# Kernel optimization log

Hardware: AMD Instinct MI355X
Metric: run time of the kernel (lower is better)

Reference implementation:

```python
import jax, jax.numpy as jnp
import numpy as np

P_W, P_H = 4, 8            # patch_size=[4,8]: p[0]=width, p[1]=height
EMBED, DEPTH, HEADS = 384, 12, 6
HD = EMBED // HEADS        # 64
THETA = 100.0
LN_EPS = 1e-5


def axial_freqs(pw, ph):
    # compute_axial_cis(dim=HD, end_x=pw, end_y=ph): angles for x and y axes, as cos/sin
    f = 1.0 / THETA ** (np.arange(0, HD, 4)[: HD // 4].astype(np.float32) / HD)  # (16,)
    t = np.arange(pw * ph, dtype=np.float32)
    tx, ty = t % pw, np.floor(t / pw)
    ang = np.concatenate([np.outer(tx, f), np.outer(ty, f)], -1)  # (N, 32)
    return jnp.asarray(np.cos(ang)), jnp.asarray(np.sin(ang))


def patchify(img):
    # (3, h, w) -> (ph*pw, 3*P_H*P_W), matching view/permute in NaViT_ROPE.forward
    c, h, w = img.shape
    ph, pw = h // P_H, w // P_W
    seq = img.reshape(c, ph, P_H, pw, P_W).transpose(1, 3, 0, 2, 4).reshape(ph * pw, -1)
    return seq, ph, pw


def layer_norm(x, w, b):
    m = x.mean(-1, keepdims=True)
    v = ((x - m) ** 2).mean(-1, keepdims=True)
    return (x - m) / jnp.sqrt(v + LN_EPS) * w + b


def rope(x, cos, sin):
    # x: (B,H,N,HD) paired as (...,HD//2,2); cos/sin: (B,N,HD//2)
    xp = x.reshape(*x.shape[:-1], -1, 2)
    x0, x1 = xp[..., 0], xp[..., 1]
    c, s = cos[:, None], sin[:, None]
    return jnp.stack([x0 * c - x1 * s, x0 * s + x1 * c], -1).reshape(x.shape)


def forward(imgs, params):
    (pe_ln_in_w, pe_ln_in_b, pe_w, pe_ln_out_w, pe_ln_out_b, blk, lnf_w, lnf_b) = params
    seqs, coss, sins, lens = [], [], [], []
    for img in imgs:
        seq, ph, pw = patchify(img)
        c, s = axial_freqs(pw, ph)
        seqs.append(seq); coss.append(c); sins.append(s); lens.append(seq.shape[0])
    nmax = max(lens)
    pad = lambda a: jnp.pad(a, ((0, nmax - a.shape[0]), (0, 0)))
    x = jnp.stack([pad(s) for s in seqs])      # (B, Nmax, 96)
    cos = jnp.stack([pad(c) for c in coss])    # (B, Nmax, 32)
    sin = jnp.stack([pad(s) for s in sins])
    mask = jnp.arange(nmax)[None, :] >= jnp.array(lens)[:, None]        # (B, Nmax), True = pad
    attn_bias = jnp.where(mask, -jnp.inf, 0.0)[:, None, None, :]        # (B,1,1,Nmax)

    # patch embed: LN(96) -> Linear(96,384,no bias) -> LN(384)
    x = layer_norm(x, pe_ln_in_w, pe_ln_in_b) @ pe_w
    x = layer_norm(x, pe_ln_out_w, pe_ln_out_b)

    scale = HD ** -0.5

    def block(x, p):
        ln1_w, ln1_b, qkv_w, qkv_b, proj_w, proj_b, ln2_w, ln2_b, fc1_w, fc1_b, fc2_w, fc2_b = p
        B, N, C = x.shape
        h = layer_norm(x, ln1_w, ln1_b)
        qkv = (h @ qkv_w + qkv_b).reshape(B, N, 3, HEADS, HD).transpose(2, 0, 3, 1, 4)
        q, k, v = qkv[0], qkv[1], qkv[2]
        q, k = rope(q, cos, sin), rope(k, cos, sin)
        attn = jnp.einsum('bhnd,bhmd->bhnm', q * scale, k) + attn_bias
        attn = jax.nn.softmax(attn, axis=-1)
        o = jnp.einsum('bhnm,bhmd->bhnd', attn, v).transpose(0, 2, 1, 3).reshape(B, N, C)
        x = x + (o @ proj_w + proj_b)
        h2 = layer_norm(x, ln2_w, ln2_b)
        h2 = jax.nn.gelu(h2 @ fc1_w + fc1_b, approximate=False)  # torch nn.GELU default (erf)
        x = x + (h2 @ fc2_w + fc2_b)
        return x, None

    x, _ = jax.lax.scan(block, x, blk)
    x = layer_norm(x, lnf_w, lnf_b)
    return x, mask


def setup_inputs() -> dict:
    key = jax.random.key(0)
    ks = jax.random.split(key, 10)
    sizes = [(3, 32, 512), (3, 32, 768), (3, 32, 896), (3, 32, 1024)]
    pd = 3 * P_H * P_W  # 96
    w = lambda k, sh: jax.random.normal(k, sh, jnp.float32) * 0.02
    inp = {}
    for i, s in enumerate(sizes):
        inp[f'img{i}'] = jax.random.normal(ks[i], s, jnp.float32)
    inp.update(
        pe_ln_in_w=jnp.ones((pd,), jnp.float32), pe_ln_in_b=jnp.zeros((pd,), jnp.float32),
        pe_w=w(ks[4], (pd, EMBED)),
        pe_ln_out_w=jnp.ones((EMBED,), jnp.float32), pe_ln_out_b=jnp.zeros((EMBED,), jnp.float32),
        ln1_w=jnp.ones((DEPTH, EMBED), jnp.float32), ln1_b=jnp.zeros((DEPTH, EMBED), jnp.float32),
        qkv_w=w(ks[5], (DEPTH, EMBED, 3 * EMBED)), qkv_b=jnp.zeros((DEPTH, 3 * EMBED), jnp.float32),
        proj_w=w(ks[6], (DEPTH, EMBED, EMBED)), proj_b=jnp.zeros((DEPTH, EMBED), jnp.float32),
        ln2_w=jnp.ones((DEPTH, EMBED), jnp.float32), ln2_b=jnp.zeros((DEPTH, EMBED), jnp.float32),
        fc1_w=w(ks[7], (DEPTH, EMBED, 4 * EMBED)), fc1_b=jnp.zeros((DEPTH, 4 * EMBED), jnp.float32),
        fc2_w=w(ks[8], (DEPTH, 4 * EMBED, EMBED)), fc2_b=jnp.zeros((DEPTH, EMBED), jnp.float32),
        lnf_w=jnp.ones((EMBED,), jnp.float32), lnf_b=jnp.zeros((EMBED,), jnp.float32),
    )
    return inp


def reference(img0, img1, img2, img3, pe_ln_in_w, pe_ln_in_b, pe_w, pe_ln_out_w, pe_ln_out_b,
              ln1_w, ln1_b, qkv_w, qkv_b, proj_w, proj_b, ln2_w, ln2_b,
              fc1_w, fc1_b, fc2_w, fc2_b, lnf_w, lnf_b):
    blk = (ln1_w, ln1_b, qkv_w, qkv_b, proj_w, proj_b, ln2_w, ln2_b, fc1_w, fc1_b, fc2_w, fc2_b)
    return forward([img0, img1, img2, img3],
                   (pe_ln_in_w, pe_ln_in_b, pe_w, pe_ln_out_w, pe_ln_out_b, blk, lnf_w, lnf_b))
```

## Files before the change

kernel.cpp:

```cpp
#include <hip/hip_runtime.h>


#define EMBED 384
#define NHEADS 6
#define HD 64
#define NSEQ 1024
#define NB 4
#define NROWS (NB * NSEQ)
#define PD 96

typedef __attribute__((ext_vector_type(8))) short bf16x8;
typedef __attribute__((ext_vector_type(4))) float f32x4;

__constant__ int c_lens[4] = {512, 768, 896, 1024};

__device__ __forceinline__ unsigned f2bf(float f) {
    unsigned u = __float_as_uint(f);
    return (u + 0x7fffu + ((u >> 16) & 1u)) >> 16;
}
__device__ __forceinline__ float bf2f(unsigned short h) {
    return __uint_as_float(((unsigned)h) << 16);
}

__global__ void patchify_kernel(const float* __restrict__ i0, const float* __restrict__ i1,
                                const float* __restrict__ i2, const float* __restrict__ i3,
                                float* __restrict__ xin, float* __restrict__ cosT,
                                float* __restrict__ sinT) {
    int bn = blockIdx.x;
    int b = bn >> 10, n = bn & 1023;
    const int lens[4] = {512, 768, 896, 1024};
    const int pws[4]  = {128, 192, 224, 256};
    const float* imgs[4] = {i0, i1, i2, i3};
    int len = lens[b], pw = pws[b];
    int W = pw * 4;
    int t = threadIdx.x;
    float* xrow = xin + (size_t)bn * PD;
    if (n < len) {
        int pr = n / pw, pc = n - pr * pw;
        const float* img = imgs[b];
        if (t < PD) {
            int c = t >> 5, py = (t >> 2) & 7, px = t & 3;
            xrow[t] = img[(size_t)c * 32 * W + (size_t)(pr * 8 + py) * W + pc * 4 + px];
        }
        if (t < 32) {
            int j = t & 15;
            float fr = powf(100.0f, -(float)j / 16.0f);
            float coord = (t < 16) ? (float)pc : (float)pr;
            float ang = coord * fr;
            cosT[(size_t)bn * 32 + t] = cosf(ang);
            sinT[(size_t)bn * 32 + t] = sinf(ang);
        }
    } else {
        if (t < PD) xrow[t] = 0.f;
        if (t < 32) { cosT[(size_t)bn * 32 + t] = 0.f; sinT[(size_t)bn * 32 + t] = 0.f; }
    }
}

__global__ void convT_kernel(const float* __restrict__ src, unsigned short* __restrict__ dst,
                             int K, int N, int Kpad) {
    __shared__ float tile[32][33];
    int k0 = blockIdx.x * 32, n0 = blockIdx.y * 32, l = blockIdx.z;
    int t = threadIdx.x;
    {
        int kk = t >> 3, nn = (t & 7) * 4;
        float4 v = make_float4(0.f, 0.f, 0.f, 0.f);
        if (k0 + kk < K)
            v = *(const float4*)(src + ((size_t)l * K + (k0 + kk)) * N + n0 + nn);
        tile[kk][nn + 0] = v.x; tile[kk][nn + 1] = v.y;
        tile[kk][nn + 2] = v.z; tile[kk][nn + 3] = v.w;
    }
    __syncthreads();
    {
        int nn = t >> 3, kk = (t & 7) * 4;
        unsigned lo = f2bf(tile[kk + 0][nn]) | (f2bf(tile[kk + 1][nn]) << 16);
        unsigned hi = f2bf(tile[kk + 2][nn]) | (f2bf(tile[kk + 3][nn]) << 16);
        uint2 u = make_uint2(lo, hi);
        *(uint2*)(dst + (size_t)l * N * Kpad + (size_t)(n0 + nn) * Kpad + k0 + kk) = u;
    }
}

template <int C, int OS, bool OBF>
__global__ void ln_kernel(const float* __restrict__ in, const float* __restrict__ w,
                          const float* __restrict__ bias, void* __restrict__ outv) {
    int row = blockIdx.x * 4 + (threadIdx.x >> 6);
    int t = threadIdx.x & 63;
    const float* x = in + (size_t)row * C;
    constexpr int NE = (C + 63) / 64;
    float vals[NE];
    float s = 0.f;
#pragma unroll
    for (int i = 0; i < NE; i++) {
        int e = t + i * 64;
        float v = (e < C) ? x[e] : 0.f;
        vals[i] = v; s += v;
    }
#pragma unroll
    for (int off = 32; off; off >>= 1) s += __shfl_down(s, off);
    float mean = __shfl(s, 0) / (float)C;
    float vs = 0.f;
#pragma unroll
    for (int i = 0; i < NE; i++) {
        int e = t + i * 64;
        float d = (e < C) ? (vals[i] - mean) : 0.f;
        vs += d * d;
    }
#pragma unroll
    for (int off = 32; off; off >>= 1) vs += __shfl_down(vs, off);
    float rstd = rsqrtf(__shfl(vs, 0) / (float)C + 1e-5f);
    constexpr int NO = (OS + 63) / 64;
#pragma unroll
    for (int i = 0; i < NO; i++) {
        int e = t + i * 64;
        if (e < OS) {
            float v = (e < C) ? ((vals[i] - mean) * rstd * w[e] + bias[e]) : 0.f;
            if (OBF) ((unsigned short*)outv)[(size_t)row * OS + e] = (unsigned short)f2bf(v);
            else     ((float*)outv)[(size_t)row * OS + e] = v;
        }
    }
}

template <int FLAGS>
__global__ __launch_bounds__(256) void gemm_bf16(
    const unsigned short* __restrict__ A, const unsigned short* __restrict__ Wt,
    const float* __restrict__ bias, const float* __restrict__ res,
    float* __restrict__ outf, unsigned short* __restrict__ outb,
    int M, int K, int N) {
    __shared__ unsigned short As[64][72];
    __shared__ unsigned short Bs[64][72];
    int t = threadIdx.x;
    int wid = t >> 6, lane = t & 63;
    int m0 = blockIdx.y * 64, n0 = blockIdx.x * 64;
    int wm = (wid >> 1) * 32, wn = (wid & 1) * 32;
    f32x4 acc[2][2] = {};
    int srow = t >> 2, sc = (t & 3) * 8;
    const unsigned short* Ap = A + (size_t)(m0 + srow) * K + sc;
    const unsigned short* Bp = Wt + (size_t)(n0 + srow) * K + sc;
    int lr = lane & 15, lk = (lane >> 4) * 8;
    for (int k0 = 0; k0 < K; k0 += 64) {
        *(uint4*)&As[srow][sc]      = *(const uint4*)(Ap + k0);
        *(uint4*)&As[srow][sc + 32] = *(const uint4*)(Ap + k0 + 32);
        *(uint4*)&Bs[srow][sc]      = *(const uint4*)(Bp + k0);
        *(uint4*)&Bs[srow][sc + 32] = *(const uint4*)(Bp + k0 + 32);
        __syncthreads();
#pragma unroll
        for (int kk = 0; kk < 64; kk += 32) {
            bf16x8 a0 = *(const bf16x8*)&As[wm + lr][kk + lk];
            bf16x8 a1 = *(const bf16x8*)&As[wm + 16 + lr][kk + lk];
            bf16x8 b0 = *(const bf16x8*)&Bs[wn + lr][kk + lk];
            bf16x8 b1 = *(const bf16x8*)&Bs[wn + 16 + lr][kk + lk];
            acc[0][0] = __builtin_amdgcn_mfma_f32_16x16x32_bf16(a0, b0, acc[0][0], 0, 0, 0);
            acc[0][1] = __builtin_amdgcn_mfma_f32_16x16x32_bf16(a0, b1, acc[0][1], 0, 0, 0);
            acc[1][0] = __builtin_amdgcn_mfma_f32_16x16x32_bf16(a1, b0, acc[1][0], 0, 0, 0);
            acc[1][1] = __builtin_amdgcn_mfma_f32_16x16x32_bf16(a1, b1, acc[1][1], 0, 0, 0);
        }
        __syncthreads();
    }
    int lq = lane >> 4;
#pragma unroll
    for (int mi = 0; mi < 2; mi++)
#pragma unroll
        for (int ni = 0; ni < 2; ni++) {
#pragma unroll
            for (int r = 0; r < 4; r++) {
                int grow = m0 + wm + mi * 16 + lq * 4 + r;
                int gcol = n0 + wn + ni * 16 + lr;
                float v = acc[mi][ni][r];
                if (FLAGS & 1) v += bias[gcol];
                if (FLAGS & 2) v = 0.5f * v * (1.f + erff(v * 0.70710678118654752f));
                if (FLAGS & 4) v += res[(size_t)grow * N + gcol];
                if (FLAGS & 8) outb[(size_t)grow * N + gcol] = (unsigned short)f2bf(v);
                else           outf[(size_t)grow * N + gcol] = v;
            }
        }
}

template <int FLAGS>
__global__ __launch_bounds__(256) void gemm_bf16_128(
    const unsigned short* __restrict__ A, const unsigned short* __restrict__ Wt,
    const float* __restrict__ bias, const float* __restrict__ res,
    float* __restrict__ outf, unsigned short* __restrict__ outb,
    int M, int K, int N) {
    __shared__ unsigned short As[128][72];
    __shared__ unsigned short Bs[128][72];
    int t = threadIdx.x;
    int wid = t >> 6, lane = t & 63;
    int m0 = blockIdx.y * 128, n0 = blockIdx.x * 128;
    int wm = (wid >> 1) * 64, wn = (wid & 1) * 64;
    f32x4 acc[4][4] = {};
    int srow = t >> 3, sc = (t & 7) * 8;
    const unsigned short* Ap = A + (size_t)(m0 + srow) * K + sc;
    const unsigned short* Bp = Wt + (size_t)(n0 + srow) * K + sc;
    int lr = lane & 15, lk = (lane >> 4) * 8;
    for (int k0 = 0; k0 < K; k0 += 64) {
#pragma unroll
        for (int rr = 0; rr < 4; rr++) {
            *(uint4*)&As[srow + rr * 32][sc] = *(const uint4*)(Ap + (size_t)(rr * 32) * K + k0);
            *(uint4*)&Bs[srow + rr * 32][sc] = *(const uint4*)(Bp + (size_t)(rr * 32) * K + k0);
        }
        __syncthreads();
#pragma unroll
        for (int kk = 0; kk < 64; kk += 32) {
            bf16x8 af[4], bfr[4];
#pragma unroll
            for (int i = 0; i < 4; i++) af[i]  = *(const bf16x8*)&As[wm + i * 16 + lr][kk + lk];
#pragma unroll
            for (int j = 0; j < 4; j++) bfr[j] = *(const bf16x8*)&Bs[wn + j * 16 + lr][kk + lk];
#pragma unroll
            for (int i = 0; i < 4; i++)
#pragma unroll
                for (int j = 0; j < 4; j++)
                    acc[i][j] = __builtin_amdgcn_mfma_f32_16x16x32_bf16(af[i], bfr[j], acc[i][j], 0, 0, 0);
        }
        __syncthreads();
    }
    int lq = lane >> 4;
#pragma unroll
    for (int mi = 0; mi < 4; mi++)
#pragma unroll
        for (int ni = 0; ni < 4; ni++) {
#pragma unroll
            for (int r = 0; r < 4; r++) {
                int grow = m0 + wm + mi * 16 + lq * 4 + r;
                int gcol = n0 + wn + ni * 16 + lr;
                float v = acc[mi][ni][r];
                if (FLAGS & 1) v += bias[gcol];
                if (FLAGS & 2) v = 0.5f * v * (1.f + erff(v * 0.70710678118654752f));
                if (FLAGS & 4) v += res[(size_t)grow * N + gcol];
                if (FLAGS & 8) outb[(size_t)grow * N + gcol] = (unsigned short)f2bf(v);
                else           outf[(size_t)grow * N + gcol] = v;
            }
        }
}

__global__ __launch_bounds__(256) void gemm_qkv_rope(
    const unsigned short* __restrict__ A, const unsigned short* __restrict__ Wt,
    const float* __restrict__ bias, const float* __restrict__ cosT,
    const float* __restrict__ sinT, unsigned short* __restrict__ qr,
    unsigned short* __restrict__ kr, unsigned short* __restrict__ vt) {
    const int K = 384;
    __shared__ unsigned short As[64][72];
    __shared__ unsigned short Bs[64][72];
    int t = threadIdx.x;
    int wid = t >> 6, lane = t & 63;
    int m0 = blockIdx.y * 64, n0 = blockIdx.x * 64;
    int wm = (wid >> 1) * 32, wn = (wid & 1) * 32;
    f32x4 acc[2][2] = {};
    int srow = t >> 2, sc = (t & 3) * 8;
    const unsigned short* Ap = A + (size_t)(m0 + srow) * K + sc;
    const unsigned short* Bp = Wt + (size_t)(n0 + srow) * K + sc;
    int lr = lane & 15, lk = (lane >> 4) * 8;
    for (int k0 = 0; k0 < K; k0 += 64) {
        *(uint4*)&As[srow][sc]      = *(const uint4*)(Ap + k0);
        *(uint4*)&As[srow][sc + 32] = *(const uint4*)(Ap + k0 + 32);
        *(uint4*)&Bs[srow][sc]      = *(const uint4*)(Bp + k0);
        *(uint4*)&Bs[srow][sc + 32] = *(const uint4*)(Bp + k0 + 32);
        __syncthreads();
#pragma unroll
        for (int kk = 0; kk < 64; kk += 32) {
            bf16x8 a0 = *(const bf16x8*)&As[wm + lr][kk + lk];
            bf16x8 a1 = *(const bf16x8*)&As[wm + 16 + lr][kk + lk];
            bf16x8 b0 = *(const bf16x8*)&Bs[wn + lr][kk + lk];
            bf16x8 b1 = *(const bf16x8*)&Bs[wn + 16 + lr][kk + lk];
            acc[0][0] = __builtin_amdgcn_mfma_f32_16x16x32_bf16(a0, b0, acc[0][0], 0, 0, 0);
            acc[0][1] = __builtin_amdgcn_mfma_f32_16x16x32_bf16(a0, b1, acc[0][1], 0, 0, 0);
            acc[1][0] = __builtin_amdgcn_mfma_f32_16x16x32_bf16(a1, b0, acc[1][0], 0, 0, 0);
            acc[1][1] = __builtin_amdgcn_mfma_f32_16x16x32_bf16(a1, b1, acc[1][1], 0, 0, 0);
        }
        __syncthreads();
    }
    int lq = lane >> 4;
    int bx = blockIdx.x;
    int sec = bx / 6, hh = bx - sec * 6;
    if (sec == 2) {
#pragma unroll
        for (int mi = 0; mi < 2; mi++)
#pragma unroll
            for (int ni = 0; ni < 2; ni++) {
                int d = wn + ni * 16 + lr;
                float bb = bias[768 + hh * 64 + d];
                int g0 = m0 + wm + mi * 16 + lq * 4;
                int b = g0 >> 10, n = g0 & 1023;
                uint2 u;
                u.x = f2bf(acc[mi][ni][0] + bb) | (f2bf(acc[mi][ni][1] + bb) << 16);
                u.y = f2bf(acc[mi][ni][2] + bb) | (f2bf(acc[mi][ni][3] + bb) << 16);
                *(uint2*)&vt[((size_t)(b * 6 + hh) * HD + d) * NSEQ + n] = u;
            }
    } else {
        unsigned short* dst = sec ? kr : qr;
        float scl = sec ? 1.0f : 0.125f;
#pragma unroll
        for (int mi = 0; mi < 2; mi++)
#pragma unroll
            for (int ni = 0; ni < 2; ni++) {
                int d = wn + ni * 16 + lr;
                float bb = bias[sec * 384 + hh * 64 + d];
                int pp = d >> 1;
#pragma unroll
                for (int r = 0; r < 4; r++) {
                    int grow = m0 + wm + mi * 16 + lq * 4 + r;
                    float v = acc[mi][ni][r] + bb;
                    float c = cosT[(size_t)grow * 32 + pp];
                    float s = sinT[(size_t)grow * 32 + pp];
                    float vp = __shfl_xor(v, 1);
                    float out = ((d & 1) == 0 ? v * c - vp * s : vp * s + v * c) * scl;
                    int b = grow >> 10, n = grow & 1023;
                    dst[((size_t)(b * 6 + hh) * NSEQ + n) * HD + d] = (unsigned short)f2bf(out);
                }
            }
    }
}

__global__ __launch_bounds__(256) void attn_mfma(
    const unsigned short* __restrict__ qr, const unsigned short* __restrict__ kr,
    const unsigned short* __restrict__ vt, unsigned short* __restrict__ opart,
    float* __restrict__ mP, float* __restrict__ lP) {
    __shared__ unsigned short Ks[64][72];
    __shared__ unsigned short Vs[64][72];
    __shared__ unsigned short Pb[4][16][72];
    __shared__ float Aw[4][16];
    int bh = blockIdx.x;
    int q0 = blockIdx.y * 64;
    int z  = blockIdx.z;
    int len = c_lens[bh / 6];
    int T = len >> 6;
    int t0 = (T * z) >> 2, t1 = (T * (z + 1)) >> 2;
    int t = threadIdx.x, wid = t >> 6, lane = t & 63;
    int lz = lane & 15, lq = lane >> 4;
    const unsigned short* Qp = qr + ((size_t)bh * NSEQ + q0 + wid * 16 + lz) * HD + lq * 8;
    bf16x8 qa0 = *(const bf16x8*)(Qp);
    bf16x8 qa1 = *(const bf16x8*)(Qp + 32);
    int srow = t >> 2, sc = (t & 3) * 16;
    const unsigned short* Kp = kr + (size_t)bh * NSEQ * HD + (size_t)srow * HD + sc;
    const unsigned short* Vp = vt + ((size_t)bh * HD + srow) * NSEQ + sc;
    f32x4 oacc[4] = {};
    float m_s = -1e30f, l_s = 0.f;
    for (int kt = t0; kt < t1; kt++) {
        int k0 = kt << 6;
        __syncthreads();
        *(uint4*)&Ks[srow][sc]     = *(const uint4*)(Kp + (size_t)k0 * HD);
        *(uint4*)&Ks[srow][sc + 8] = *(const uint4*)(Kp + (size_t)k0 * HD + 8);
        *(uint4*)&Vs[srow][sc]     = *(const uint4*)(Vp + k0);
        *(uint4*)&Vs[srow][sc + 8] = *(const uint4*)(Vp + k0 + 8);
        __syncthreads();
        f32x4 s[4] = {};
#pragma unroll
        for (int g = 0; g < 4; g++) {
            bf16x8 kf0 = *(const bf16x8*)&Ks[g * 16 + lz][lq * 8];
            bf16x8 kf1 = *(const bf16x8*)&Ks[g * 16 + lz][32 + lq * 8];
            s[g] = __builtin_amdgcn_mfma_f32_16x16x32_bf16(kf0, qa0, s[g], 0, 0, 0);
            s[g] = __builtin_amdgcn_mfma_f32_16x16x32_bf16(kf1, qa1, s[g], 0, 0, 0);
        }
        float mx = s[0][0];
#pragma unroll
        for (int g = 0; g < 4; g++)
#pragma unroll
            for (int r = 0; r < 4; r++) mx = fmaxf(mx, s[g][r]);
        mx = fmaxf(mx, __shfl_xor(mx, 16));
        mx = fmaxf(mx, __shfl_xor(mx, 32));
        float mn = fmaxf(m_s, mx);
        float a_s = __expf(m_s - mn);
        m_s = mn;
        float sum = 0.f;
#pragma unroll
        for (int g = 0; g < 4; g++)
#pragma unroll
            for (int r = 0; r < 4; r++) {
                float p = __expf(s[g][r] - mn);
                s[g][r] = p;
                sum += p;
            }
        sum += __shfl_xor(sum, 16);
        sum += __shfl_xor(sum, 32);
        l_s = l_s * a_s + sum;
        if (lq == 0) Aw[wid][lz] = a_s;
#pragma unroll
        for (int g = 0; g < 4; g++) {
            uint2 u;
            u.x = f2bf(s[g][0]) | (f2bf(s[g][1]) << 16);
            u.y = f2bf(s[g][2]) | (f2bf(s[g][3]) << 16);
            *(uint2*)&Pb[wid][lz][g * 16 + lq * 4] = u;
        }
        f32x4 al4 = *(const f32x4*)&Aw[wid][lq * 4];
        bf16x8 pa0 = *(const bf16x8*)&Pb[wid][lz][lq * 8];
        bf16x8 pa1 = *(const bf16x8*)&Pb[wid][lz][32 + lq * 8];
#pragma unroll
        for (int g = 0; g < 4; g++) {
#pragma unroll
            for (int r = 0; r < 4; r++) oacc[g][r] *= al4[r];
            bf16x8 vf0 = *(const bf16x8*)&Vs[g * 16 + lz][lq * 8];
            bf16x8 vf1 = *(const bf16x8*)&Vs[g * 16 + lz][32 + lq * 8];
            oacc[g] = __builtin_amdgcn_mfma_f32_16x16x32_bf16(pa0, vf0, oacc[g], 0, 0, 0);
            oacc[g] = __builtin_amdgcn_mfma_f32_16x16x32_bf16(pa1, vf1, oacc[g], 0, 0, 0);
        }
    }
    size_t rb = ((size_t)z * 24 + bh) * NSEQ + q0 + wid * 16;
    if (lq == 0) { mP[rb + lz] = m_s; lP[rb + lz] = l_s; }
#pragma unroll
    for (int r = 0; r < 4; r++) {
        int row = lq * 4 + r;
#pragma unroll
        for (int g = 0; g < 4; g++)
            opart[(rb + row) * HD + g * 16 + lz] = (unsigned short)f2bf(oacc[g][r]);
    }
}

__global__ void attn_combine(const unsigned short* __restrict__ opart,
                             const float* __restrict__ mP, const float* __restrict__ lP,
                             unsigned short* __restrict__ o) {
    int idx = blockIdx.x * 4 + (threadIdx.x >> 6);
    int lane = threadIdx.x & 63;
    int bh = idx >> 10, n = idx & 1023;
    int b = bh / 6, hh = bh - b * 6;
    float m[4], l[4];
#pragma unroll
    for (int z = 0; z < 4; z++) {
        m[z] = mP[((size_t)z * 24 + bh) * NSEQ + n];
        l[z] = lP[((size_t)z * 24 + bh) * NSEQ + n];
    }
    float ms = fmaxf(fmaxf(m[0], m[1]), fmaxf(m[2], m[3]));
    float ls = 0.f, w[4];
#pragma unroll
    for (int z = 0; z < 4; z++) { w[z] = __expf(m[z] - ms); ls += l[z] * w[z]; }
    float inv = 1.f / ls;
    float acc = 0.f;
#pragma unroll
    for (int z = 0; z < 4; z++)
        acc += bf2f(opart[(((size_t)z * 24 + bh) * NSEQ + n) * HD + lane]) * w[z];
    o[((size_t)b * NSEQ + n) * EMBED + hh * HD + lane] = (unsigned short)f2bf(acc * inv);
}

__global__ void mask_kernel(float* __restrict__ mout) {
    int idx = blockIdx.x * 256 + threadIdx.x;
    if (idx >= NROWS) return;
    int b = idx >> 10, n = idx & 1023;
    mout[idx] = (n >= c_lens[b]) ? 1.0f : 0.0f;
}

extern "C" void kernel_launch(void* const* d_in, const int* in_sizes, int n_in,
                              void* d_out, int out_size, void* d_ws, size_t ws_size,
                              hipStream_t stream) {
    (void)in_sizes; (void)n_in; (void)out_size; (void)ws_size;
    const float* img0 = (const float*)d_in[0];
    const float* img1 = (const float*)d_in[1];
    const float* img2 = (const float*)d_in[2];
    const float* img3 = (const float*)d_in[3];
    const float* pe_ln_in_w  = (const float*)d_in[4];
    const float* pe_ln_in_b  = (const float*)d_in[5];
    const float* pe_w        = (const float*)d_in[6];
    const float* pe_ln_out_w = (const float*)d_in[7];
    const float* pe_ln_out_b = (const float*)d_in[8];
    const float* ln1_w  = (const float*)d_in[9];
    const float* ln1_b  = (const float*)d_in[10];
    const float* qkv_w  = (const float*)d_in[11];
    const float* qkv_b  = (const float*)d_in[12];
    const float* proj_w = (const float*)d_in[13];
    const float* proj_b = (const float*)d_in[14];
    const float* ln2_w  = (const float*)d_in[15];
    const float* ln2_b  = (const float*)d_in[16];
    const float* fc1_w  = (const float*)d_in[17];
    const float* fc1_b  = (const float*)d_in[18];
    const float* fc2_w  = (const float*)d_in[19];
    const float* fc2_b  = (const float*)d_in[20];
    const float* lnf_w  = (const float*)d_in[21];
    const float* lnf_b  = (const float*)d_in[22];

    char* ws = (char*)d_ws;
    float*          x_f    = (float*)(ws + 0);
    char*           R      = ws + 6291456;
    unsigned short* opart  = (unsigned short*)R;
    unsigned short* mlp_bf = (unsigned short*)R;
    unsigned short* h_bf   = (unsigned short*)(ws + 18874368);
    unsigned short* o_bf   = h_bf;
    unsigned short* qr     = (unsigned short*)(ws + 22020096);
    unsigned short* kr     = (unsigned short*)(ws + 25165824);
    unsigned short* vt     = (unsigned short*)(ws + 28311552);
    float*          cosT   = (float*)(ws + 31457280);
    float*          sinT   = (float*)(ws + 31981568);
    float*          xin    = (float*)(ws + 32505856);
    float*          mPt    = xin;
    float*          lPt    = (float*)(ws + 32505856 + 393216);
    unsigned short* xln_bf = (unsigned short*)(ws + 34078720);
    unsigned short* pe_wt  = (unsigned short*)(ws + 35127296);
    unsigned short* qkv_wt = (unsigned short*)(ws + 35225600);
    unsigned short* proj_wt= (unsigned short*)(ws + 45842432);
    unsigned short* fc1_wt = (unsigned short*)(ws + 49381376);
    unsigned short* fc2_wt = (unsigned short*)(ws + 63537152);

    convT_kernel<<<dim3(4, 12, 1),   256, 0, stream>>>(pe_w,   pe_wt,   96,  EMBED, 128);
    convT_kernel<<<dim3(12, 36, 12), 256, 0, stream>>>(qkv_w,  qkv_wt,  384, 1152,  384);
    convT_kernel<<<dim3(12, 12, 12), 256, 0, stream>>>(proj_w, proj_wt, 384, 384,   384);
    convT_kernel<<<dim3(12, 48, 12), 256, 0, stream>>>(fc1_w,  fc1_wt,  384, 1536,  384);
    convT_kernel<<<dim3(48, 12, 12), 256, 0, stream>>>(fc2_w,  fc2_wt,  1536, 384,  1536);

    patchify_kernel<<<NROWS, 128, 0, stream>>>(img0, img1, img2, img3, xin, cosT, sinT);
    ln_kernel<PD, 128, true><<<NROWS / 4, 256, 0, stream>>>(xin, pe_ln_in_w, pe_ln_in_b, xln_bf);
    gemm_bf16<0><<<dim3(EMBED / 64, NROWS / 64), 256, 0, stream>>>(
        xln_bf, pe_wt, nullptr, nullptr, x_f, nullptr, NROWS, 128, EMBED);
    ln_kernel<EMBED, EMBED, false><<<NROWS / 4, 256, 0, stream>>>(x_f, pe_ln_out_w, pe_ln_out_b, x_f);

    for (int l = 0; l < 12; ++l) {
        ln_kernel<EMBED, EMBED, true><<<NROWS / 4, 256, 0, stream>>>(
            x_f, ln1_w + l * EMBED, ln1_b + l * EMBED, h_bf);
        gemm_qkv_rope<<<dim3(18, NROWS / 64), 256, 0, stream>>>(
            h_bf, qkv_wt + (size_t)l * 1152 * 384, qkv_b + (size_t)l * 1152,
            cosT, sinT, qr, kr, vt);
        attn_mfma<<<dim3(NB * NHEADS, NSEQ / 64, 4), 256, 0, stream>>>(
            qr, kr, vt, opart, mPt, lPt);
        attn_combine<<<NB * NHEADS * NSEQ / 4, 256, 0, stream>>>(opart, mPt, lPt, o_bf);
        gemm_bf16<5><<<dim3(EMBED / 64, NROWS / 64), 256, 0, stream>>>(
            o_bf, proj_wt + (size_t)l * 384 * 384, proj_b + (size_t)l * EMBED, x_f,
            x_f, nullptr, NROWS, EMBED, EMBED);
        ln_kernel<EMBED, EMBED, true><<<NROWS / 4, 256, 0, stream>>>(
            x_f, ln2_w + l * EMBED, ln2_b + l * EMBED, h_bf);
        gemm_bf16_128<11><<<dim3(1536 / 128, NROWS / 128), 256, 0, stream>>>(
            h_bf, fc1_wt + (size_t)l * 1536 * 384, fc1_b + (size_t)l * 1536, nullptr,
            nullptr, mlp_bf, NROWS, EMBED, 1536);
        gemm_bf16<5><<<dim3(EMBED / 64, NROWS / 64), 256, 0, stream>>>(
            mlp_bf, fc2_wt + (size_t)l * 384 * 1536, fc2_b + (size_t)l * EMBED, x_f,
            x_f, nullptr, NROWS, 1536, EMBED);
    }

    ln_kernel<EMBED, EMBED, false><<<NROWS / 4, 256, 0, stream>>>(x_f, lnf_w, lnf_b, (float*)d_out);
    mask_kernel<<<16, 256, 0, stream>>>((float*)d_out + (size_t)NROWS * EMBED);
}
```

Baseline: 1.262 ms.

## Use direct global-to-LDS loads and 128x128 tiles for QKV and FC1 GEMMs

```diff
diff --git a/kernel.cpp b/kernel.cpp
--- a/kernel.cpp
+++ b/kernel.cpp
@@ -21,6 +21,10 @@
 __device__ __forceinline__ float bf2f(unsigned short h) {
     return __uint_as_float(((unsigned)h) << 16);
 }
+
+#define GLOAD16(gp, lp) __builtin_amdgcn_global_load_lds( \
+    (const __attribute__((address_space(1))) unsigned int*)(gp), \
+    (__attribute__((address_space(3))) unsigned int*)(lp), 16, 0, 0)
 
 __global__ void patchify_kernel(const float* __restrict__ i0, const float* __restrict__ i1,
                                 const float* __restrict__ i2, const float* __restrict__ i3,
@@ -175,43 +179,49 @@
 }
 
 template <int FLAGS>
-__global__ __launch_bounds__(256) void gemm_bf16_128(
+__global__ __launch_bounds__(256) void gemm128_glds(
     const unsigned short* __restrict__ A, const unsigned short* __restrict__ Wt,
     const float* __restrict__ bias, const float* __restrict__ res,
     float* __restrict__ outf, unsigned short* __restrict__ outb,
     int M, int K, int N) {
-    __shared__ unsigned short As[128][72];
-    __shared__ unsigned short Bs[128][72];
+    __shared__ unsigned short As[128 * 64];
+    __shared__ unsigned short Bs[128 * 64];
     int t = threadIdx.x;
     int wid = t >> 6, lane = t & 63;
     int m0 = blockIdx.y * 128, n0 = blockIdx.x * 128;
     int wm = (wid >> 1) * 64, wn = (wid & 1) * 64;
     f32x4 acc[4][4] = {};
-    int srow = t >> 3, sc = (t & 7) * 8;
-    const unsigned short* Ap = A + (size_t)(m0 + srow) * K + sc;
-    const unsigned short* Bp = Wt + (size_t)(n0 + srow) * K + sc;
+    int srow = wid * 32 + (lane >> 3);
+    int scol = (lane & 7) * 8;
+    const unsigned short* Ag = A + (size_t)(m0 + srow) * K + scol;
+    const unsigned short* Bg = Wt + (size_t)(n0 + srow) * K + scol;
+    unsigned short* Al = As + wid * 32 * 64;
+    unsigned short* Bl = Bs + wid * 32 * 64;
     int lr = lane & 15, lk = (lane >> 4) * 8;
     for (int k0 = 0; k0 < K; k0 += 64) {
-#pragma unroll
-        for (int rr = 0; rr < 4; rr++) {
-            *(uint4*)&As[srow + rr * 32][sc] = *(const uint4*)(Ap + (size_t)(rr * 32) * K + k0);
-            *(uint4*)&Bs[srow + rr * 32][sc] = *(const uint4*)(Bp + (size_t)(rr * 32) * K + k0);
-        }
+        __syncthreads();
+        GLOAD16(Ag + k0,                Al);
+        GLOAD16(Ag + (size_t)8  * K + k0, Al + 8 * 64);
+        GLOAD16(Ag + (size_t)16 * K + k0, Al + 16 * 64);
+        GLOAD16(Ag + (size_t)24 * K + k0, Al + 24 * 64);
+        GLOAD16(Bg + k0,                Bl);
+        GLOAD16(Bg + (size_t)8  * K + k0, Bl + 8 * 64);
+        GLOAD16(Bg + (size_t)16 * K + k0, Bl + 16 * 64);
+        GLOAD16(Bg + (size_t)24 * K + k0, Bl + 24 * 64);
         __syncthreads();
 #pragma unroll
         for (int kk = 0; kk < 64; kk += 32) {
             bf16x8 af[4], bfr[4];
 #pragma unroll
-            for (int i = 0; i < 4; i++) af[i]  = *(const bf16x8*)&As[wm + i * 16 + lr][kk + lk];
-#pragma unroll
-            for (int j = 0; j < 4; j++) bfr[j] = *(const bf16x8*)&Bs[wn + j * 16 + lr][kk + lk];
+            for (int i = 0; i < 4; i++) af[i]  = *(const bf16x8*)&As[(wm + i * 16 + lr) * 64 + kk + lk];
+#pragma unroll
+            for (int j = 0; j < 4; j++) bfr[j] = *(const bf16x8*)&Bs[(wn + j * 16 + lr) * 64 + kk + lk];
 #pragma unroll
             for (int i = 0; i < 4; i++)
 #pragma unroll
                 for (int j = 0; j < 4; j++)
                     acc[i][j] = __builtin_amdgcn_mfma_f32_16x16x32_bf16(af[i], bfr[j], acc[i][j], 0, 0, 0);
         }
-        __syncthreads();
     }
     int lq = lane >> 4;
 #pragma unroll
@@ -232,52 +242,62 @@
         }
 }
 
-__global__ __launch_bounds__(256) void gemm_qkv_rope(
+__global__ __launch_bounds__(256) void gemm128_qkv_rope(
     const unsigned short* __restrict__ A, const unsigned short* __restrict__ Wt,
     const float* __restrict__ bias, const float* __restrict__ cosT,
     const float* __restrict__ sinT, unsigned short* __restrict__ qr,
     unsigned short* __restrict__ kr, unsigned short* __restrict__ vt) {
     const int K = 384;
-    __shared__ unsigned short As[64][72];
-    __shared__ unsigned short Bs[64][72];
+    __shared__ unsigned short As[128 * 64];
+    __shared__ unsigned short Bs[128 * 64];
     int t = threadIdx.x;
     int wid = t >> 6, lane = t & 63;
-    int m0 = blockIdx.y * 64, n0 = blockIdx.x * 64;
-    int wm = (wid >> 1) * 32, wn = (wid & 1) * 32;
-    f32x4 acc[2][2] = {};
-    int srow = t >> 2, sc = (t & 3) * 8;
-    const unsigned short* Ap = A + (size_t)(m0 + srow) * K + sc;
-    const unsigned short* Bp = Wt + (size_t)(n0 + srow) * K + sc;
+    int m0 = blockIdx.y * 128, n0 = blockIdx.x * 128;
+    int wm = (wid >> 1) * 64, wn = (wid & 1) * 64;
+    f32x4 acc[4][4] = {};
+    int srow = wid * 32 + (lane >> 3);
+    int scol = (lane & 7) * 8;
+    const unsigned short* Ag = A + (size_t)(m0 + srow) * K + scol;
+    const unsigned short* Bg = Wt + (size_t)(n0 + srow) * K + scol;
+    unsigned short* Al = As + wid * 32 * 64;
+    unsigned short* Bl = Bs + wid * 32 * 64;
     int lr = lane & 15, lk = (lane >> 4) * 8;
     for (int k0 = 0; k0 < K; k0 += 64) {
-        *(uint4*)&As[srow][sc]      = *(const uint4*)(Ap + k0);
-        *(uint4*)&As[srow][sc + 32] = *(const uint4*)(Ap + k0 + 32);
-        *(uint4*)&Bs[srow][sc]      = *(const uint4*)(Bp + k0);
-        *(uint4*)&Bs[srow][sc + 32] = *(const uint4*)(Bp + k0 + 32);
+        __syncthreads();
+        GLOAD16(Ag + k0,                Al);
+        GLOAD16(Ag + (size_t)8  * K + k0, Al + 8 * 64);
+        GLOAD16(Ag + (size_t)16 * K + k0, Al + 16 * 64);
+        GLOAD16(Ag + (size_t)24 * K + k0, Al + 24 * 64);
+        GLOAD16(Bg + k0,                Bl);
+        GLOAD16(Bg + (size_t)8  * K + k0, Bl + 8 * 64);
+        GLOAD16(Bg + (size_t)16 * K + k0, Bl + 16 * 64);
+        GLOAD16(Bg + (size_t)24 * K + k0, Bl + 24 * 64);
         __syncthreads();
 #pragma unroll
         for (int kk = 0; kk < 64; kk += 32) {
-            bf16x8 a0 = *(const bf16x8*)&As[wm + lr][kk + lk];
-            bf16x8 a1 = *(const bf16x8*)&As[wm + 16 + lr][kk + lk];
-            bf16x8 b0 = *(const bf16x8*)&Bs[wn + lr][kk + lk];
-            bf16x8 b1 = *(const bf16x8*)&Bs[wn + 16 + lr][kk + lk];
-            acc[0][0] = __builtin_amdgcn_mfma_f32_16x16x32_bf16(a0, b0, acc[0][0], 0, 0, 0);
-            acc[0][1] = __builtin_amdgcn_mfma_f32_16x16x32_bf16(a0, b1, acc[0][1], 0, 0, 0);
-            acc[1][0] = __builtin_amdgcn_mfma_f32_16x16x32_bf16(a1, b0, acc[1][0], 0, 0, 0);
-            acc[1][1] = __builtin_amdgcn_mfma_f32_16x16x32_bf16(a1, b1, acc[1][1], 0, 0, 0);
-        }
-        __syncthreads();
+            bf16x8 af[4], bfr[4];
+#pragma unroll
+            for (int i = 0; i < 4; i++) af[i]  = *(const bf16x8*)&As[(wm + i * 16 + lr) * 64 + kk + lk];
+#pragma unroll
+            for (int j = 0; j < 4; j++) bfr[j] = *(const bf16x8*)&Bs[(wn + j * 16 + lr) * 64 + kk + lk];
+#pragma unroll
+            for (int i = 0; i < 4; i++)
+#pragma unroll
+                for (int j = 0; j < 4; j++)
+                    acc[i][j] = __builtin_amdgcn_mfma_f32_16x16x32_bf16(af[i], bfr[j], acc[i][j], 0, 0, 0);
+        }
     }
     int lq = lane >> 4;
-    int bx = blockIdx.x;
-    int sec = bx / 6, hh = bx - sec * 6;
-    if (sec == 2) {
-#pragma unroll
-        for (int mi = 0; mi < 2; mi++)
-#pragma unroll
-            for (int ni = 0; ni < 2; ni++) {
-                int d = wn + ni * 16 + lr;
-                float bb = bias[768 + hh * 64 + d];
+#pragma unroll
+    for (int ni = 0; ni < 4; ni++) {
+        int col = n0 + wn + ni * 16 + lr;
+        int sec = col / 384;
+        int wsec = col - sec * 384;
+        int hh = wsec >> 6, d = wsec & 63;
+        float bb = bias[col];
+        if (sec == 2) {
+#pragma unroll
+            for (int mi = 0; mi < 4; mi++) {
                 int g0 = m0 + wm + mi * 16 + lq * 4;
                 int b = g0 >> 10, n = g0 & 1023;
                 uint2 u;
@@ -285,16 +305,12 @@
                 u.y = f2bf(acc[mi][ni][2] + bb) | (f2bf(acc[mi][ni][3] + bb) << 16);
                 *(uint2*)&vt[((size_t)(b * 6 + hh) * HD + d) * NSEQ + n] = u;
             }
-    } else {
-        unsigned short* dst = sec ? kr : qr;
-        float scl = sec ? 1.0f : 0.125f;
-#pragma unroll
-        for (int mi = 0; mi < 2; mi++)
-#pragma unroll
-            for (int ni = 0; ni < 2; ni++) {
-                int d = wn + ni * 16 + lr;
-                float bb = bias[sec * 384 + hh * 64 + d];
-                int pp = d >> 1;
+        } else {
+            unsigned short* dst = sec ? kr : qr;
+            float scl = sec ? 1.0f : 0.125f;
+            int pp = d >> 1;
+#pragma unroll
+            for (int mi = 0; mi < 4; mi++) {
 #pragma unroll
                 for (int r = 0; r < 4; r++) {
                     int grow = m0 + wm + mi * 16 + lq * 4 + r;
@@ -307,6 +323,7 @@
                     dst[((size_t)(b * 6 + hh) * NSEQ + n) * HD + d] = (unsigned short)f2bf(out);
                 }
             }
+        }
     }
 }
 
@@ -501,7 +518,7 @@
     for (int l = 0; l < 12; ++l) {
         ln_kernel<EMBED, EMBED, true><<<NROWS / 4, 256, 0, stream>>>(
             x_f, ln1_w + l * EMBED, ln1_b + l * EMBED, h_bf);
-        gemm_qkv_rope<<<dim3(18, NROWS / 64), 256, 0, stream>>>(
+        gemm128_qkv_rope<<<dim3(1152 / 128, NROWS / 128), 256, 0, stream>>>(
             h_bf, qkv_wt + (size_t)l * 1152 * 384, qkv_b + (size_t)l * 1152,
             cosT, sinT, qr, kr, vt);
         attn_mfma<<<dim3(NB * NHEADS, NSEQ / 64, 4), 256, 0, stream>>>(
@@ -512,7 +529,7 @@
             x_f, nullptr, NROWS, EMBED, EMBED);
         ln_kernel<EMBED, EMBED, true><<<NROWS / 4, 256, 0, stream>>>(
             x_f, ln2_w + l * EMBED, ln2_b + l * EMBED, h_bf);
-        gemm_bf16_128<11><<<dim3(1536 / 128, NROWS / 128), 256, 0, stream>>>(
+        gemm128_glds<11><<<dim3(1536 / 128, NROWS / 128), 256, 0, stream>>>(
             h_bf, fc1_wt + (size_t)l * 1536 * 384, fc1_b + (size_t)l * 1536, nullptr,
             nullptr, mlp_bf, NROWS, EMBED, 1536);
         gemm_bf16<5><<<dim3(EMBED / 64, NROWS / 64), 256, 0, stream>>>(
```

New measurement: 1.423 ms. 12.7% more time.

## Fuse split-K attention combine into projection GEMM and halve KV splits

Applied to the files above, without the earlier changes.

```diff
diff --git a/kernel.cpp b/kernel.cpp
--- a/kernel.cpp
+++ b/kernel.cpp
@@ -8,6 +8,7 @@
 #define NB 4
 #define NROWS (NB * NSEQ)
 #define PD 96
+#define NZ 2
 
 typedef __attribute__((ext_vector_type(8))) short bf16x8;
 typedef __attribute__((ext_vector_type(4))) float f32x4;
@@ -323,7 +324,7 @@
     int z  = blockIdx.z;
     int len = c_lens[bh / 6];
     int T = len >> 6;
-    int t0 = (T * z) >> 2, t1 = (T * (z + 1)) >> 2;
+    int t0 = (T * z) >> 1, t1 = (T * (z + 1)) >> 1;
     int t = threadIdx.x, wid = t >> 6, lane = t & 63;
     int lz = lane & 15, lq = lane >> 4;
     const unsigned short* Qp = qr + ((size_t)bh * NSEQ + q0 + wid * 16 + lz) * HD + lq * 8;
@@ -404,29 +405,92 @@
     }
 }
 
-__global__ void attn_combine(const unsigned short* __restrict__ opart,
-                             const float* __restrict__ mP, const float* __restrict__ lP,
-                             unsigned short* __restrict__ o) {
-    int idx = blockIdx.x * 4 + (threadIdx.x >> 6);
-    int lane = threadIdx.x & 63;
-    int bh = idx >> 10, n = idx & 1023;
-    int b = bh / 6, hh = bh - b * 6;
-    float m[4], l[4];
-#pragma unroll
-    for (int z = 0; z < 4; z++) {
-        m[z] = mP[((size_t)z * 24 + bh) * NSEQ + n];
-        l[z] = lP[((size_t)z * 24 + bh) * NSEQ + n];
-    }
-    float ms = fmaxf(fmaxf(m[0], m[1]), fmaxf(m[2], m[3]));
-    float ls = 0.f, w[4];
-#pragma unroll
-    for (int z = 0; z < 4; z++) { w[z] = __expf(m[z] - ms); ls += l[z] * w[z]; }
-    float inv = 1.f / ls;
-    float acc = 0.f;
-#pragma unroll
-    for (int z = 0; z < 4; z++)
-        acc += bf2f(opart[(((size_t)z * 24 + bh) * NSEQ + n) * HD + lane]) * w[z];
-    o[((size_t)b * NSEQ + n) * EMBED + hh * HD + lane] = (unsigned short)f2bf(acc * inv);
+__global__ __launch_bounds__(256) void gemm_proj_combine(
+    const unsigned short* __restrict__ opart, const float* __restrict__ mP,
+    const float* __restrict__ lP, const unsigned short* __restrict__ Wt,
+    const float* __restrict__ bias, float* __restrict__ xio) {
+    const int K = 384, N = 384;
+    __shared__ unsigned short As[64][72];
+    __shared__ unsigned short Bs[64][72];
+    __shared__ float Winv[64][6][NZ];
+    int t = threadIdx.x;
+    int wid = t >> 6, lane = t & 63;
+    int m0 = blockIdx.y * 64, n0 = blockIdx.x * 64;
+    int wm = (wid >> 1) * 32, wn = (wid & 1) * 32;
+    const size_t zstride = (size_t)24 * NSEQ * HD;
+    for (int p = t; p < 384; p += 256) {
+        int tok = p / 6, hh = p - tok * 6;
+        int g = m0 + tok, b = g >> 10, n = g & 1023;
+        int bh = b * 6 + hh;
+        size_t i0 = (size_t)bh * NSEQ + n;
+        float ma = mP[i0], mb = mP[i0 + (size_t)24 * NSEQ];
+        float la = lP[i0], lb = lP[i0 + (size_t)24 * NSEQ];
+        float ms = fmaxf(ma, mb);
+        float wa = __expf(ma - ms), wb = __expf(mb - ms);
+        float inv = 1.f / (la * wa + lb * wb);
+        Winv[tok][hh][0] = wa * inv;
+        Winv[tok][hh][1] = wb * inv;
+    }
+    __syncthreads();
+    f32x4 acc[2][2] = {};
+    int srow = t >> 2, sc = (t & 3) * 8;
+    int gg = m0 + srow, gb = gg >> 10, gn = gg & 1023;
+    const unsigned short* Bp = Wt + (size_t)(n0 + srow) * K + sc;
+    int lr = lane & 15, lk = (lane >> 4) * 8;
+    for (int k0 = 0; k0 < K; k0 += 64) {
+#pragma unroll
+        for (int h = 0; h < 2; h++) {
+            int col = k0 + sc + h * 32;
+            int hh = col >> 6, d = col & 63;
+            int bh = gb * 6 + hh;
+            size_t base = ((size_t)bh * NSEQ + gn) * HD + d;
+            float w0 = Winv[srow][hh][0], w1 = Winv[srow][hh][1];
+            uint4 u0 = *(const uint4*)&opart[base];
+            uint4 u1 = *(const uint4*)&opart[base + zstride];
+            unsigned a[4] = {u0.x, u0.y, u0.z, u0.w};
+            unsigned c[4] = {u1.x, u1.y, u1.z, u1.w};
+            uint4 outw;
+            unsigned rr[4];
+#pragma unroll
+            for (int q = 0; q < 4; q++) {
+                float lo = bf2f((unsigned short)(a[q] & 0xffff)) * w0 +
+                           bf2f((unsigned short)(c[q] & 0xffff)) * w1;
+                float hi = bf2f((unsigned short)(a[q] >> 16)) * w0 +
+                           bf2f((unsigned short)(c[q] >> 16)) * w1;
+                rr[q] = f2bf(lo) | (f2bf(hi) << 16);
+            }
+            outw.x = rr[0]; outw.y = rr[1]; outw.z = rr[2]; outw.w = rr[3];
+            *(uint4*)&As[srow][sc + h * 32] = outw;
+        }
+        *(uint4*)&Bs[srow][sc]      = *(const uint4*)(Bp + k0);
+        *(uint4*)&Bs[srow][sc + 32] = *(const uint4*)(Bp + k0 + 32);
+        __syncthreads();
+#pragma unroll
+        for (int kk = 0; kk < 64; kk += 32) {
+            bf16x8 a0 = *(const bf16x8*)&As[wm + lr][kk + lk];
+            bf16x8 a1 = *(const bf16x8*)&As[wm + 16 + lr][kk + lk];
+            bf16x8 b0 = *(const bf16x8*)&Bs[wn + lr][kk + lk];
+            bf16x8 b1 = *(const bf16x8*)&Bs[wn + 16 + lr][kk + lk];
+            acc[0][0] = __builtin_amdgcn_mfma_f32_16x16x32_bf16(a0, b0, acc[0][0], 0, 0, 0);
+            acc[0][1] = __builtin_amdgcn_mfma_f32_16x16x32_bf16(a0, b1, acc[0][1], 0, 0, 0);
+            acc[1][0] = __builtin_amdgcn_mfma_f32_16x16x32_bf16(a1, b0, acc[1][0], 0, 0, 0);
+            acc[1][1] = __builtin_amdgcn_mfma_f32_16x16x32_bf16(a1, b1, acc[1][1], 0, 0, 0);
+        }
+        __syncthreads();
+    }
+    int lq = lane >> 4;
+#pragma unroll
+    for (int mi = 0; mi < 2; mi++)
+#pragma unroll
+        for (int ni = 0; ni < 2; ni++) {
+#pragma unroll
+            for (int r = 0; r < 4; r++) {
+                int grow = m0 + wm + mi * 16 + lq * 4 + r;
+                int gcol = n0 + wn + ni * 16 + lr;
+                float v = acc[mi][ni][r] + bias[gcol] + xio[(size_t)grow * N + gcol];
+                xio[(size_t)grow * N + gcol] = v;
+            }
+        }
 }
 
 __global__ void mask_kernel(float* __restrict__ mout) {
@@ -470,7 +534,6 @@
     unsigned short* opart  = (unsigned short*)R;
     unsigned short* mlp_bf = (unsigned short*)R;
     unsigned short* h_bf   = (unsigned short*)(ws + 18874368);
-    unsigned short* o_bf   = h_bf;
     unsigned short* qr     = (unsigned short*)(ws + 22020096);
     unsigned short* kr     = (unsigned short*)(ws + 25165824);
     unsigned short* vt     = (unsigned short*)(ws + 28311552);
@@ -504,19 +567,18 @@
         gemm_qkv_rope<<<dim3(18, NROWS / 64), 256, 0, stream>>>(
             h_bf, qkv_wt + (size_t)l * 1152 * 384, qkv_b + (size_t)l * 1152,
             cosT, sinT, qr, kr, vt);
-        attn_mfma<<<dim3(NB * NHEADS, NSEQ / 64, 4), 256, 0, stream>>>(
+        attn_mfma<<<dim3(NB * NHEADS, NSEQ / 64, NZ), 256, 0, stream>>>(
             qr, kr, vt, opart, mPt, lPt);
-        attn_combine<<<NB * NHEADS * NSEQ / 4, 256, 0, stream>>>(opart, mPt, lPt, o_bf);
-        gemm_bf16<5><<<dim3(EMBED / 64, NROWS / 64), 256, 0, stream>>>(
-            o_bf, proj_wt + (size_t)l * 384 * 384, proj_b + (size_t)l * EMBED, x_f,
-            x_f, nullptr, NROWS, EMBED, EMBED);
+        gemm_proj_combine<<<dim3(EMBED / 64, NROWS / 64), 256, 0, stream>>>(
+            opart, mPt, lPt, proj_wt + (size_t)l * 384 * 384,
+            proj_b + (size_t)l * EMBED, x_f);
         ln_kernel<EMBED, EMBED, true><<<NROWS / 4, 256, 0, stream>>>(
             x_f, ln2_w + l * EMBED, ln2_b + l * EMBED, h_bf);
         gemm_bf16_128<11><<<dim3(1536 / 128, NROWS / 128), 256, 0, stream>>>(
             h_bf, fc1_wt + (size_t)l * 1536 * 384, fc1_b + (size_t)l * 1536, nullptr,
             nullptr, mlp_bf, NROWS, EMBED, 1536);
         gemm_bf16<5><<<dim3(EMBED / 64, NROWS / 64), 256, 0, stream>>>(
-            mlp_bf, fc2_wt + (size_t)l * 384 * 1536, fc2_b + (size_t)l * EMBED, x_f,
+            mlp_bf, fc2_wt + (size_t)l * 1536 * 384, fc2_b + (size_t)l * EMBED, x_f,
             x_f, nullptr, NROWS, 1536, EMBED);
     }
 
```

Result: faster. 1.167 ms (-7.6%).
